# Optimization experiments

Measured on AMD Instinct MI355X. Metric: run time of the kernel, lower is better.

## Reference

```python
import jax, jax.numpy as jnp
import numpy as np
from jax import lax

B = 16384
D_MODEL = 84
N_EXPERTS = 2
TOP_K = 2
HIDDEN = 2048


def _conv(x, w, b):
    # x: [N,C,H,W], w: [O,I,kh,kw] (torch OIHW), VALID padding, stride 1
    y = lax.conv_general_dilated(x, w, (1, 1), 'VALID',
                                 dimension_numbers=('NCHW', 'OIHW', 'NCHW'))
    return y + b[None, :, None, None]


def _maxpool2(x):
    return lax.reduce_window(x, -jnp.inf, lax.max,
                             (1, 1, 2, 2), (1, 1, 2, 2), 'VALID')


def setup_inputs() -> dict:
    key = jax.random.key(0)
    ks = jax.random.split(key, 17)
    s = 0.05
    return {
        'x': jax.random.normal(ks[0], (B, 3, 32, 32), jnp.float32),
        'conv1_w': jax.random.normal(ks[1], (6, 3, 5, 5), jnp.float32) * s,
        'conv1_b': jax.random.normal(ks[2], (6,), jnp.float32) * s,
        'conv2_w': jax.random.normal(ks[3], (16, 6, 5, 5), jnp.float32) * s,
        'conv2_b': jax.random.normal(ks[4], (16,), jnp.float32) * s,
        'fc1_w': jax.random.normal(ks[5], (400, 120), jnp.float32) * s,
        'fc1_b': jax.random.normal(ks[6], (120,), jnp.float32) * s,
        'fc2_w': jax.random.normal(ks[7], (120, 84), jnp.float32) * s,
        'fc2_b': jax.random.normal(ks[8], (84,), jnp.float32) * s,
        'gate_w': jax.random.normal(ks[9], (D_MODEL, N_EXPERTS), jnp.float32) * s,
        'exp_w1': jax.random.normal(ks[10], (N_EXPERTS, D_MODEL, HIDDEN), jnp.float32) * s,
        'exp_b1': jax.random.normal(ks[11], (N_EXPERTS, HIDDEN), jnp.float32) * s,
        'exp_w2': jax.random.normal(ks[12], (N_EXPERTS, HIDDEN, D_MODEL), jnp.float32) * s,
        'exp_b2': jax.random.normal(ks[13], (N_EXPERTS, D_MODEL), jnp.float32) * s,
        'fc3_w': jax.random.normal(ks[14], (84, 10), jnp.float32) * s,
        'fc3_b': jax.random.normal(ks[15], (10,), jnp.float32) * s,
    }


def _moe(x, gate_w, exp_w1, exp_b1, exp_w2, exp_b2):
    # tutel top-k gate: softmax over expert logits, select top-k, renormalize
    n = x.shape[0]
    scores = jax.nn.softmax(x @ gate_w, axis=-1)          # [N,E]
    top_v, top_i = lax.top_k(scores, TOP_K)               # [N,k]
    gates = top_v / jnp.sum(top_v, axis=-1, keepdims=True)
    # dense combine weights [N,E] (zero where not routed)
    comb = jnp.zeros((n, N_EXPERTS), x.dtype).at[
        jnp.arange(n)[:, None], top_i].set(gates)
    # grouped expert FFN (E=2: evaluate both, weight-combine)
    h = jax.nn.relu(jnp.einsum('nd,edh->enh', x, exp_w1) + exp_b1[:, None, :])
    y = jnp.einsum('enh,ehd->end', h, exp_w2) + exp_b2[:, None, :]  # [E,N,D]
    return jnp.einsum('ne,end->nd', comb, y)


def reference(x, conv1_w, conv1_b, conv2_w, conv2_b, fc1_w, fc1_b,
              fc2_w, fc2_b, gate_w, exp_w1, exp_b1, exp_w2, exp_b2,
              fc3_w, fc3_b):
    h = _maxpool2(jax.nn.relu(_conv(x, conv1_w, conv1_b)))   # [B,6,14,14]
    h = _maxpool2(jax.nn.relu(_conv(h, conv2_w, conv2_b)))   # [B,16,5,5]
    h = h.reshape(-1, 16 * 5 * 5)                            # [B,400]
    h = jax.nn.relu(h @ fc1_w + fc1_b)                       # [B,120]
    h = jax.nn.relu(h @ fc2_w + fc2_b)                       # [B,84]
    h = _moe(h, gate_w, exp_w1, exp_b1, exp_w2, exp_b2)      # [B,84]
    return h @ fc3_w + fc3_b                                 # [B,10]
```

## Files before the change

### kernel.cpp

```cpp
#include <hip/hip_runtime.h>
#include <stdint.h>

typedef unsigned short u16;
typedef __attribute__((ext_vector_type(8))) short s8v;
typedef __attribute__((ext_vector_type(4))) float f4v;
typedef __fp16 h2v __attribute__((ext_vector_type(2)));

__device__ __forceinline__ float bu2f(u16 u) {
  return __uint_as_float(((uint32_t)u) << 16);
}
__device__ __forceinline__ u16 f2bu(float f) {
  uint32_t u = __float_as_uint(f);
  u += 0x7fffu + ((u >> 16) & 1u);
  return (u16)(u >> 16);
}

union U32H2 { uint32_t u; h2v h; };

__device__ __forceinline__ uint32_t pk2h(float a, float b) {
  U32H2 x;
  x.h = __builtin_amdgcn_cvt_pkrtz(a, b);
  return x.u;
}

__device__ __forceinline__ float fdot2u(uint32_t a, uint32_t b, float c) {
  float d;
  asm("v_dot2_f32_f16 %0, %1, %2, %3" : "=v"(d) : "v"(a), "v"(b), "v"(c));
  return d;
}

template <bool F32> struct In;
template <> struct In<true> {
  static __device__ __forceinline__ float ld(const void* p, long i) {
    return ((const float*)p)[i];
  }
};
template <> struct In<false> {
  static __device__ __forceinline__ float ld(const void* p, long i) {
    return bu2f(((const u16*)p)[i]);
  }
};

__global__ void k_detect(const u16* __restrict__ x, int* __restrict__ flag) {
  __shared__ int s[64];
  int cnt = 0;
  for (int i = threadIdx.x; i < 2048; i += 64) {
    int e = (x[i] >> 7) & 0xFF;
    cnt += (e >= 96 && e <= 134) ? 1 : 0;
  }
  s[threadIdx.x] = cnt;
  __syncthreads();
  if (threadIdx.x == 0) {
    int t = 0;
    for (int i = 0; i < 64; ++i) t += s[i];
    *flag = (t >= 1843) ? 0 : 1;
  }
}

__device__ __forceinline__ u16 f2h16(float f) {
  __fp16 h = (__fp16)f;
  u16 r;
  __builtin_memcpy(&r, &h, 2);
  return r;
}

template <bool INF32>
__global__ __launch_bounds__(256) void k_trans(
    const int* __restrict__ flag,
    const void* __restrict__ fc1w, const void* __restrict__ fc2w,
    const void* __restrict__ ew1, const void* __restrict__ ew2,
    const void* __restrict__ c1w, const void* __restrict__ c1b,
    const void* __restrict__ c2w, const void* __restrict__ c2b,
    u16* __restrict__ fc1t, u16* __restrict__ fc2t,
    u16* __restrict__ w1t, u16* __restrict__ w2t,
    uint32_t* __restrict__ cdw) {
  if (*flag != (INF32 ? 1 : 0)) return;
  long gid = (long)blockIdx.x * 256 + threadIdx.x;
  if (gid < 53248) {
    int n = (int)(gid / 416), k = (int)(gid % 416);
    fc1t[gid] = (n < 120 && k < 400) ? f2bu(In<INF32>::ld(fc1w, (long)k * 120 + n)) : (u16)0;
  } else if (gid < 65536) {
    long i = gid - 53248;
    int n = (int)(i / 128), k = (int)(i % 128);
    fc2t[i] = (n < 84 && k < 120) ? f2bu(In<INF32>::ld(fc2w, (long)k * 84 + n)) : (u16)0;
  } else if (gid < 458752) {
    long i = gid - 65536;
    int e = (int)(i / 196608);
    long r = i % 196608;
    int n = (int)(r / 96), k = (int)(r % 96);
    w1t[i] = (k < 84) ? f2bu(In<INF32>::ld(ew1, ((long)e * 84 + k) * 2048 + n)) : (u16)0;
  } else if (gid < 851968) {
    long i = gid - 458752;
    int e = (int)(i / 196608);
    long r = i % 196608;
    int n = (int)(r / 2048), k = (int)(r % 2048);
    w2t[i] = (n < 84) ? f2bu(In<INF32>::ld(ew2, ((long)e * 2048 + k) * 84 + n)) : (u16)0;
  } else if (gid < 853700) {
    long i = gid - 851968;
    if (i < 270) {
      int p = (int)(i % 3), ky = (int)((i / 3) % 5);
      int ic = (int)((i / 15) % 3), c = (int)(i / 45);
      long base = (((long)c * 3 + ic) * 5 + ky) * 5;
      float w0 = In<INF32>::ld(c1w, base + 2 * p);
      float w1 = (2 * p + 1 < 5) ? In<INF32>::ld(c1w, base + 2 * p + 1) : 0.f;
      cdw[i] = (uint32_t)f2h16(w0) | ((uint32_t)f2h16(w1) << 16);
    } else if (i < 1710) {
      long j = i - 270;
      int p = (int)(j % 3), ky = (int)((j / 3) % 5);
      int ic = (int)((j / 15) % 6), c = (int)(j / 90);
      long base = (((long)c * 6 + ic) * 5 + ky) * 5;
      float w0 = In<INF32>::ld(c2w, base + 2 * p);
      float w1 = (2 * p + 1 < 5) ? In<INF32>::ld(c2w, base + 2 * p + 1) : 0.f;
      cdw[270 + j] = (uint32_t)f2h16(w0) | ((uint32_t)f2h16(w1) << 16);
    } else if (i < 1716) {
      ((float*)(cdw + 1710))[i - 1710] = In<INF32>::ld(c1b, i - 1710);
    } else if (i < 1732) {
      ((float*)(cdw + 1716))[i - 1716] = In<INF32>::ld(c2b, i - 1716);
    }
  }
}

#define CIMG 5
template <bool INF32>
__global__ __launch_bounds__(256) void k_conv(
    const int* __restrict__ flag,
    const void* __restrict__ x,
    const uint32_t* __restrict__ cdw,
    u16* __restrict__ p2, int Btot) {
  if (*flag != (INF32 ? 1 : 0)) return;
  __shared__ u16 sxh[CIMG * 3 * 32 * 36];
  __shared__ u16 sp1h[CIMG * 6 * 14 * 18];
  const uint32_t* cd1 = cdw;
  const uint32_t* cd2 = cdw + 270;
  const float* cb1 = (const float*)(cdw + 1710);
  const float* cb2 = (const float*)(cdw + 1716);
  const int tid = threadIdx.x;
  const long gimg0 = (long)blockIdx.x * CIMG;

  for (int r = tid; r < CIMG * 96; r += 256) {
    *(uint32_t*)(sxh + (size_t)r * 36 + 32) = 0;
    *(uint32_t*)(sxh + (size_t)r * 36 + 34) = 0;
  }
  for (int r = tid; r < CIMG * 84; r += 256) {
    *(uint32_t*)(sp1h + (size_t)r * 18 + 14) = 0;
    *(uint32_t*)(sp1h + (size_t)r * 18 + 16) = 0;
  }

  for (int i = tid; i < CIMG * 96; i += 256) {
    int img = i / 96, rem = i - img * 96;
    if (gimg0 + img < Btot) {
      long goff = (gimg0 + img) * 3072 + (long)rem * 32;
      u16* dst = sxh + (size_t)i * 36;
      if (!INF32) {
        const uint32_t* src = (const uint32_t*)((const u16*)x + goff);
#pragma unroll
        for (int j = 0; j < 16; ++j) {
          uint32_t d = src[j];
          *(uint32_t*)(dst + 2 * j) =
              pk2h(__uint_as_float(d << 16), __uint_as_float(d & 0xffff0000u));
        }
      } else {
        const float* src = (const float*)x + goff;
#pragma unroll
        for (int j = 0; j < 16; ++j)
          *(uint32_t*)(dst + 2 * j) = pk2h(src[2 * j], src[2 * j + 1]);
      }
    }
  }
  __syncthreads();

  for (int task = tid; task < CIMG * 196; task += 256) {
    int img = task / 196, pos = task - img * 196;
    if (gimg0 + img >= Btot) continue;
    int py = pos / 14, px = pos - py * 14;
    int x0 = 2 * px, y0 = 2 * py;
    float acc[6][4];
#pragma unroll
    for (int c = 0; c < 6; ++c) {
      float bv = cb1[c];
      acc[c][0] = bv; acc[c][1] = bv; acc[c][2] = bv; acc[c][3] = bv;
    }
    for (int ic = 0; ic < 3; ++ic) {
      uint32_t A[6][4], S[6][3];
      const u16* rb = sxh + ((size_t)(img * 3 + ic) * 32 + y0) * 36 + x0;
#pragma unroll
      for (int r = 0; r < 6; ++r) {
#pragma unroll
        for (int p = 0; p < 4; ++p)
          A[r][p] = *(const uint32_t*)(rb + (size_t)r * 36 + 2 * p);
#pragma unroll
        for (int p = 0; p < 3; ++p)
          S[r][p] = (A[r][p] >> 16) | (A[r][p + 1] << 16);
      }
#pragma unroll
      for (int c = 0; c < 6; ++c) {
        const uint32_t* wb = cd1 + ((c * 3 + ic) * 5) * 3;
#pragma unroll
        for (int ky = 0; ky < 5; ++ky) {
#pragma unroll
          for (int p = 0; p < 3; ++p) {
            uint32_t w = wb[ky * 3 + p];
            acc[c][0] = fdot2u(A[ky][p], w, acc[c][0]);
            acc[c][1] = fdot2u(S[ky][p], w, acc[c][1]);
            acc[c][2] = fdot2u(A[ky + 1][p], w, acc[c][2]);
            acc[c][3] = fdot2u(S[ky + 1][p], w, acc[c][3]);
          }
        }
      }
    }
#pragma unroll
    for (int c = 0; c < 6; ++c) {
      float m = fmaxf(0.f, fmaxf(fmaxf(acc[c][0], acc[c][1]),
                                 fmaxf(acc[c][2], acc[c][3])));
      sp1h[((size_t)(img * 6 + c) * 14 + py) * 18 + px] = f2h16(m);
    }
  }
  __syncthreads();

  for (int task = tid; task < CIMG * 100; task += 256) {
    int img = task / 100, r0 = task - img * 100;
    if (gimg0 + img >= Btot) continue;
    int grp = r0 / 25, pos = r0 - grp * 25;
    int py = pos / 5, px = pos - py * 5;
    int x0 = 2 * px, y0 = 2 * py;
    int c0 = grp * 4;
    float acc[4][4];
#pragma unroll
    for (int c = 0; c < 4; ++c) {
      float bv = cb2[c0 + c];
      acc[c][0] = bv; acc[c][1] = bv; acc[c][2] = bv; acc[c][3] = bv;
    }
    for (int ic = 0; ic < 6; ++ic) {
      uint32_t A[6][4], S[6][3];
      const u16* rb = sp1h + ((size_t)(img * 6 + ic) * 14 + y0) * 18 + x0;
#pragma unroll
      for (int r = 0; r < 6; ++r) {
#pragma unroll
        for (int p = 0; p < 4; ++p)
          A[r][p] = *(const uint32_t*)(rb + (size_t)r * 18 + 2 * p);
#pragma unroll
        for (int p = 0; p < 3; ++p)
          S[r][p] = (A[r][p] >> 16) | (A[r][p + 1] << 16);
      }
#pragma unroll
      for (int c = 0; c < 4; ++c) {
        const uint32_t* wb = cd2 + (((c0 + c) * 6 + ic) * 5) * 3;
#pragma unroll
        for (int ky = 0; ky < 5; ++ky) {
#pragma unroll
          for (int p = 0; p < 3; ++p) {
            uint32_t w = wb[ky * 3 + p];
            acc[c][0] = fdot2u(A[ky][p], w, acc[c][0]);
            acc[c][1] = fdot2u(S[ky][p], w, acc[c][1]);
            acc[c][2] = fdot2u(A[ky + 1][p], w, acc[c][2]);
            acc[c][3] = fdot2u(S[ky + 1][p], w, acc[c][3]);
          }
        }
      }
    }
    u16* pout = p2 + (gimg0 + img) * 416;
#pragma unroll
    for (int c = 0; c < 4; ++c) {
      float m = fmaxf(0.f, fmaxf(fmaxf(acc[c][0], acc[c][1]),
                                 fmaxf(acc[c][2], acc[c][3])));
      pout[(c0 + c) * 25 + py * 5 + px] = f2bu(m);
    }
  }

  for (int i = tid; i < CIMG * 16; i += 256) {
    int img = i / 16;
    if (gimg0 + img < Btot) p2[(gimg0 + img) * 416 + 400 + (i & 15)] = 0;
  }
}

template <bool INF32>
__global__ __launch_bounds__(256) void k_fcA(
    const int* __restrict__ flag,
    const u16* __restrict__ p2,
    const u16* __restrict__ fc1t, const u16* __restrict__ fc2t,
    const void* __restrict__ fc1b, const void* __restrict__ fc2b,
    const void* __restrict__ gw,
    u16* __restrict__ a2buf, float* __restrict__ scbuf) {
  if (*flag != (INF32 ? 1 : 0)) return;
  __shared__ __align__(16) char smem[62976];
  u16* a2s = (u16*)smem;
  u16* hs = (u16*)(smem + 13312);
  u16* wbuf = (u16*)(smem + 31232);
  u16* xs = (u16*)(smem + 57856);

  const int tid = threadIdx.x;
  const int wv = tid >> 6, ln = tid & 63;
  const int m = ln & 15, quad = ln >> 4;
  const long t0 = (long)blockIdx.x * 64;
  const int row0 = wv * 16 + quad * 4;

  for (int i = tid; i < 30720 / 4; i += 256) ((uint32_t*)smem)[i] = 0;

  f4v acc1[8];
#pragma unroll
  for (int i = 0; i < 8; ++i) acc1[i] = (f4v){0.f, 0.f, 0.f, 0.f};
  for (int s = 0; s < 13; ++s) {
    {
      int r = tid >> 2, c0 = (tid & 3) * 8;
      *(uint4*)(xs + r * 40 + c0) =
          *(const uint4*)(p2 + (t0 + r) * 416 + s * 32 + c0);
      int n = tid >> 1, cw = (tid & 1) * 16;
      *(uint4*)(wbuf + n * 40 + cw) = *(const uint4*)(fc1t + (long)n * 416 + s * 32 + cw);
      *(uint4*)(wbuf + n * 40 + cw + 8) =
          *(const uint4*)(fc1t + (long)n * 416 + s * 32 + cw + 8);
    }
    __syncthreads();
    s8v a = *(const s8v*)(xs + (wv * 16 + m) * 40 + quad * 8);
#pragma unroll
    for (int nt = 0; nt < 8; ++nt) {
      s8v b = *(const s8v*)(wbuf + (nt * 16 + m) * 40 + quad * 8);
      acc1[nt] = __builtin_amdgcn_mfma_f32_16x16x32_bf16(a, b, acc1[nt], 0, 0, 0);
    }
    __syncthreads();
  }
#pragma unroll
  for (int nt = 0; nt < 8; ++nt) {
    int n = nt * 16 + m;
    if (n < 120) {
      float bv = In<INF32>::ld(fc1b, n);
#pragma unroll
      for (int r = 0; r < 4; ++r)
        hs[(row0 + r) * 136 + n] = f2bu(fmaxf(acc1[nt][r] + bv, 0.f));
    }
  }
  __syncthreads();

  for (int i = tid; i < 1536; i += 256) {
    int n = i >> 4, c0 = (i & 15) * 8;
    *(uint4*)(wbuf + n * 136 + c0) = *(const uint4*)(fc2t + n * 128 + c0);
  }
  __syncthreads();
  f4v acc2[6];
#pragma unroll
  for (int i = 0; i < 6; ++i) acc2[i] = (f4v){0.f, 0.f, 0.f, 0.f};
  for (int s = 0; s < 4; ++s) {
    s8v a = *(const s8v*)(hs + (wv * 16 + m) * 136 + s * 32 + quad * 8);
#pragma unroll
    for (int nt = 0; nt < 6; ++nt) {
      s8v b = *(const s8v*)(wbuf + (nt * 16 + m) * 136 + s * 32 + quad * 8);
      acc2[nt] = __builtin_amdgcn_mfma_f32_16x16x32_bf16(a, b, acc2[nt], 0, 0, 0);
    }
  }
  __syncthreads();
#pragma unroll
  for (int nt = 0; nt < 6; ++nt) {
    int n = nt * 16 + m;
    if (n < 84) {
      float bv = In<INF32>::ld(fc2b, n);
#pragma unroll
      for (int r = 0; r < 4; ++r)
        a2s[(row0 + r) * 104 + n] = f2bu(fmaxf(acc2[nt][r] + bv, 0.f));
    }
  }
  __syncthreads();

  if (tid < 64) {
    const u16* xr = a2s + tid * 104;
    float l0 = 0.f, l1 = 0.f;
    for (int k = 0; k < 84; ++k) {
      float xv = bu2f(xr[k]);
      l0 = fmaf(xv, In<INF32>::ld(gw, 2 * k), l0);
      l1 = fmaf(xv, In<INF32>::ld(gw, 2 * k + 1), l1);
    }
    float mx = fmaxf(l0, l1);
    float e0 = __expf(l0 - mx), e1 = __expf(l1 - mx);
    float inv = 1.f / (e0 + e1);
    *(float2*)(scbuf + (t0 + tid) * 2) = make_float2(e0 * inv, e1 * inv);
  }
  for (int i = tid; i < 832; i += 256) {
    int r = i / 13, c0 = (i - r * 13) * 8;
    *(uint4*)(a2buf + (t0 + r) * 104 + c0) = *(const uint4*)(a2s + r * 104 + c0);
  }
}

template <bool INF32>
__global__ __launch_bounds__(256) void k_exp(
    const int* __restrict__ flag,
    const u16* __restrict__ a2buf, const float* __restrict__ scbuf,
    const u16* __restrict__ w1t, const u16* __restrict__ w2t,
    const void* __restrict__ eb1, const void* __restrict__ eb2,
    float* __restrict__ ybuf, int Btok) {
  if (*flag != (INF32 ? 1 : 0)) return;
  __shared__ __align__(16) char smem[57856];
  u16* a2s = (u16*)smem;
  u16* hs = (u16*)(smem + 13312);
  u16* wbuf = (u16*)(smem + 30720);
  float* scs = (float*)(smem + 57344);

  const int tid = threadIdx.x;
  const int wv = tid >> 6, ln = tid & 63;
  const int m = ln & 15, quad = ln >> 4;
  const int e = blockIdx.y;
  const long t0 = (long)blockIdx.x * 64;
  const int row0 = wv * 16 + quad * 4;
  const u16* w1te = w1t + (long)e * 196608;
  const u16* w2te = w2t + (long)e * 196608;

  for (int i = tid; i < 832; i += 256) {
    int r = i / 13, c0 = (i - r * 13) * 8;
    *(uint4*)(a2s + r * 104 + c0) = *(const uint4*)(a2buf + (t0 + r) * 104 + c0);
  }
  if (tid < 64) scs[tid] = scbuf[(t0 + tid) * 2 + e];
  __syncthreads();

  f4v acce[6];
#pragma unroll
  for (int i = 0; i < 6; ++i) acce[i] = (f4v){0.f, 0.f, 0.f, 0.f};
  for (int c = 0; c < 16; ++c) {
    const int n0 = c * 128;
    if (c) __syncthreads();
    for (int i = tid; i < 1536; i += 256) {
      int nl = i / 12, c0 = (i - nl * 12) * 8;
      *(uint4*)(wbuf + nl * 104 + c0) =
          *(const uint4*)(w1te + (long)(n0 + nl) * 96 + c0);
    }
    __syncthreads();
    f4v acch[8];
#pragma unroll
    for (int i = 0; i < 8; ++i) acch[i] = (f4v){0.f, 0.f, 0.f, 0.f};
    for (int s = 0; s < 3; ++s) {
      s8v a = *(const s8v*)(a2s + (wv * 16 + m) * 104 + s * 32 + quad * 8);
#pragma unroll
      for (int nt = 0; nt < 8; ++nt) {
        s8v b = *(const s8v*)(wbuf + (nt * 16 + m) * 104 + s * 32 + quad * 8);
        acch[nt] = __builtin_amdgcn_mfma_f32_16x16x32_bf16(a, b, acch[nt], 0, 0, 0);
      }
    }
#pragma unroll
    for (int nt = 0; nt < 8; ++nt) {
      float bv = In<INF32>::ld(eb1, (long)e * 2048 + n0 + nt * 16 + m);
#pragma unroll
      for (int r = 0; r < 4; ++r)
        hs[(row0 + r) * 136 + nt * 16 + m] = f2bu(fmaxf(acch[nt][r] + bv, 0.f));
    }
    __syncthreads();
    for (int i = tid; i < 1536; i += 256) {
      int n = i >> 4, c0 = (i & 15) * 8;
      *(uint4*)(wbuf + n * 136 + c0) =
          *(const uint4*)(w2te + (long)n * 2048 + n0 + c0);
    }
    __syncthreads();
    for (int s = 0; s < 4; ++s) {
      s8v a = *(const s8v*)(hs + (wv * 16 + m) * 136 + s * 32 + quad * 8);
#pragma unroll
      for (int nt = 0; nt < 6; ++nt) {
        s8v b = *(const s8v*)(wbuf + (nt * 16 + m) * 136 + s * 32 + quad * 8);
        acce[nt] = __builtin_amdgcn_mfma_f32_16x16x32_bf16(a, b, acce[nt], 0, 0, 0);
      }
    }
  }

#pragma unroll
  for (int nt = 0; nt < 6; ++nt) {
    int d = nt * 16 + m;
    float bv = (d < 84) ? In<INF32>::ld(eb2, (long)e * 84 + d) : 0.f;
#pragma unroll
    for (int r = 0; r < 4; ++r) {
      float sc = scs[row0 + r];
      ybuf[((size_t)e * Btok + t0 + row0 + r) * 96 + d] = sc * (acce[nt][r] + bv);
    }
  }
}

template <bool INF32>
__global__ __launch_bounds__(256) void k_fc3(
    const int* __restrict__ flag,
    const float* __restrict__ ybuf,
    const void* __restrict__ w3, const void* __restrict__ b3,
    void* __restrict__ out, int Btok) {
  if (*flag != (INF32 ? 1 : 0)) return;
  __shared__ float sw3[840];
  __shared__ float sb3[10];
  const int tid = threadIdx.x;
  const long t0 = (long)blockIdx.x * 64;
  for (int i = tid; i < 840; i += 256) sw3[i] = In<INF32>::ld(w3, i);
  if (tid < 10) sb3[tid] = In<INF32>::ld(b3, tid);
  __syncthreads();
  for (int idx = tid; idx < 640; idx += 256) {
    int tk = idx / 10, cc = idx - tk * 10;
    const float* y0r = ybuf + (t0 + tk) * 96;
    const float* y1r = ybuf + ((size_t)Btok + t0 + tk) * 96;
    float acc = sb3[cc];
    for (int d = 0; d < 84; ++d)
      acc = fmaf(y0r[d] + y1r[d], sw3[d * 10 + cc], acc);
    long oi = (t0 + tk) * 10 + cc;
    if (INF32) ((float*)out)[oi] = acc;
    else ((u16*)out)[oi] = f2bu(acc);
  }
}

extern "C" void kernel_launch(void* const* d_in, const int* in_sizes, int n_in,
                              void* d_out, int out_size, void* d_ws, size_t ws_size,
                              hipStream_t stream) {
  const int B = in_sizes[0] / 3072;
  char* wsb = (char*)d_ws;
  int* flag = (int*)wsb;
  u16* p2 = (u16*)(wsb + 64);
  u16* fc1t = p2 + (size_t)B * 416;
  u16* fc2t = fc1t + 53248;
  u16* w1t = fc2t + 12288;
  u16* w2t = w1t + 393216;
  uint32_t* cdw = (uint32_t*)(w2t + 393216);
  u16* a2buf = (u16*)(cdw + 1732);
  float* scbuf = (float*)(a2buf + (size_t)B * 104);
  float* ybuf = scbuf + (size_t)B * 2;

  k_detect<<<1, 64, 0, stream>>>((const u16*)d_in[0], flag);

  k_trans<false><<<3336, 256, 0, stream>>>(flag, d_in[5], d_in[7], d_in[10],
                                           d_in[12], d_in[1], d_in[2], d_in[3],
                                           d_in[4], fc1t, fc2t, w1t, w2t, cdw);
  k_trans<true><<<3336, 256, 0, stream>>>(flag, d_in[5], d_in[7], d_in[10],
                                          d_in[12], d_in[1], d_in[2], d_in[3],
                                          d_in[4], fc1t, fc2t, w1t, w2t, cdw);

  const int convGrid = (B + CIMG - 1) / CIMG;
  k_conv<false><<<convGrid, 256, 0, stream>>>(flag, d_in[0], cdw, p2, B);
  k_conv<true><<<convGrid, 256, 0, stream>>>(flag, d_in[0], cdw, p2, B);

  k_fcA<false><<<B / 64, 256, 0, stream>>>(flag, p2, fc1t, fc2t, d_in[6],
                                           d_in[8], d_in[9], a2buf, scbuf);
  k_fcA<true><<<B / 64, 256, 0, stream>>>(flag, p2, fc1t, fc2t, d_in[6],
                                          d_in[8], d_in[9], a2buf, scbuf);

  dim3 eg(B / 64, 2);
  k_exp<false><<<eg, 256, 0, stream>>>(flag, a2buf, scbuf, w1t, w2t, d_in[11],
                                       d_in[13], ybuf, B);
  k_exp<true><<<eg, 256, 0, stream>>>(flag, a2buf, scbuf, w1t, w2t, d_in[11],
                                      d_in[13], ybuf, B);

  k_fc3<false><<<B / 64, 256, 0, stream>>>(flag, ybuf, d_in[14], d_in[15],
                                           d_out, B);
  k_fc3<true><<<B / 64, 256, 0, stream>>>(flag, ybuf, d_in[14], d_in[15],
                                          d_out, B);
}
```

Baseline: 621.2 us.

## Move conv1/conv2 from dot2 FMA loops to 16x16x32 f16 MFMA

Both conv layers are recast as small GEMMs on the 16x16x32 f16 MFMA, replacing the v_dot2 scalar accumulation. Each pooled output's 4 window positions map to MFMA rows, so the max-pool becomes a reduction over the accumulator lanes. Weights are repacked into a padded MFMA B-fragment layout, and inputs are stored twice in LDS (normal and shifted by one element) so odd-x windows can be fetched with aligned 32-bit loads. This trades doubled LDS footprint and a smaller images-per-block count (5 to 4) for far fewer VALU instructions in the conv stage, which likely dominates runtime.

```diff
diff --git a/kernel.cpp b/kernel.cpp
--- a/kernel.cpp
+++ b/kernel.cpp
@@ -5,6 +5,7 @@
 typedef __attribute__((ext_vector_type(8))) short s8v;
 typedef __attribute__((ext_vector_type(4))) float f4v;
 typedef __fp16 h2v __attribute__((ext_vector_type(2)));
+typedef __fp16 h8v __attribute__((ext_vector_type(8)));
 
 __device__ __forceinline__ float bu2f(u16 u) {
   return __uint_as_float(((uint32_t)u) << 16);
@@ -21,12 +22,6 @@
   U32H2 x;
   x.h = __builtin_amdgcn_cvt_pkrtz(a, b);
   return x.u;
-}
-
-__device__ __forceinline__ float fdot2u(uint32_t a, uint32_t b, float c) {
-  float d;
-  asm("v_dot2_f32_f16 %0, %1, %2, %3" : "=v"(d) : "v"(a), "v"(b), "v"(c));
-  return d;
 }
 
 template <bool F32> struct In;
@@ -95,32 +90,37 @@
     long r = i % 196608;
     int n = (int)(r / 2048), k = (int)(r % 2048);
     w2t[i] = (n < 84) ? f2bu(In<INF32>::ld(ew2, ((long)e * 2048 + k) * 84 + n)) : (u16)0;
-  } else if (gid < 853700) {
+  } else if (gid < 856598) {
     long i = gid - 851968;
-    if (i < 270) {
-      int p = (int)(i % 3), ky = (int)((i / 3) % 5);
-      int ic = (int)((i / 15) % 3), c = (int)(i / 45);
-      long base = (((long)c * 3 + ic) * 5 + ky) * 5;
-      float w0 = In<INF32>::ld(c1w, base + 2 * p);
-      float w1 = (2 * p + 1 < 5) ? In<INF32>::ld(c1w, base + 2 * p + 1) : 0.f;
-      cdw[i] = (uint32_t)f2h16(w0) | ((uint32_t)f2h16(w1) << 16);
-    } else if (i < 1710) {
-      long j = i - 270;
-      int p = (int)(j % 3), ky = (int)((j / 3) % 5);
-      int ic = (int)((j / 15) % 6), c = (int)(j / 90);
-      long base = (((long)c * 6 + ic) * 5 + ky) * 5;
-      float w0 = In<INF32>::ld(c2w, base + 2 * p);
-      float w1 = (2 * p + 1 < 5) ? In<INF32>::ld(c2w, base + 2 * p + 1) : 0.f;
-      cdw[270 + j] = (uint32_t)f2h16(w0) | ((uint32_t)f2h16(w1) << 16);
-    } else if (i < 1716) {
-      ((float*)(cdw + 1710))[i - 1710] = In<INF32>::ld(c1b, i - 1710);
-    } else if (i < 1732) {
-      ((float*)(cdw + 1716))[i - 1716] = In<INF32>::ld(c2b, i - 1716);
-    }
-  }
-}
-
-#define CIMG 5
+    u16* cdh = (u16*)cdw;
+    if (i < 1536) {
+      int ic = (int)(i >> 9);
+      int r = (int)(i & 511);
+      int lnn = r >> 3, j = r & 7;
+      int n = lnn & 15, qd = lnn >> 4;
+      int t = qd * 8 + j, ky = t / 6, kxp = t - ky * 6;
+      float v = (n < 6 && t < 30 && kxp < 5)
+          ? In<INF32>::ld(c1w, ((long)(n * 3 + ic) * 5 + ky) * 5 + kxp) : 0.f;
+      cdh[i] = f2h16(v);
+    } else if (i < 4608) {
+      long jj = i - 1536;
+      int ic = (int)(jj >> 9);
+      int r = (int)(jj & 511);
+      int lnn = r >> 3, j = r & 7;
+      int n = lnn & 15, qd = lnn >> 4;
+      int t = qd * 8 + j, ky = t / 6, kxp = t - ky * 6;
+      float v = (t < 30 && kxp < 5)
+          ? In<INF32>::ld(c2w, ((long)(n * 6 + ic) * 5 + ky) * 5 + kxp) : 0.f;
+      cdh[1536 + jj] = f2h16(v);
+    } else if (i < 4614) {
+      ((float*)(cdw + 2304))[i - 4608] = In<INF32>::ld(c1b, i - 4608);
+    } else if (i < 4630) {
+      ((float*)(cdw + 2310))[i - 4614] = In<INF32>::ld(c2b, i - 4614);
+    }
+  }
+}
+
+#define CIMG 4
 template <bool INF32>
 __global__ __launch_bounds__(256) void k_conv(
     const int* __restrict__ flag,
@@ -128,143 +128,140 @@
     const uint32_t* __restrict__ cdw,
     u16* __restrict__ p2, int Btot) {
   if (*flag != (INF32 ? 1 : 0)) return;
-  __shared__ u16 sxh[CIMG * 3 * 32 * 36];
-  __shared__ u16 sp1h[CIMG * 6 * 14 * 18];
-  const uint32_t* cd1 = cdw;
-  const uint32_t* cd2 = cdw + 270;
-  const float* cb1 = (const float*)(cdw + 1710);
-  const float* cb2 = (const float*)(cdw + 1716);
+  __shared__ __align__(16) u16 sxn[CIMG * 3 * 32 * 36];
+  __shared__ __align__(16) u16 sxs[CIMG * 3 * 32 * 36];
+  __shared__ __align__(16) u16 sp1n[CIMG * 6 * 14 * 18];
+  __shared__ __align__(16) u16 sp1s[CIMG * 6 * 14 * 18];
+  __shared__ u16 lut1[196];
+  __shared__ u16 lut2[32];
+  const u16* cdh = (const u16*)cdw;
+  const float* cb1f = (const float*)(cdw + 2304);
+  const float* cb2f = (const float*)(cdw + 2310);
   const int tid = threadIdx.x;
+  const int wv = tid >> 6, ln = tid & 63;
+  const int mrow = ln & 15, quad = ln >> 4;
   const long gimg0 = (long)blockIdx.x * CIMG;
 
-  for (int r = tid; r < CIMG * 96; r += 256) {
-    *(uint32_t*)(sxh + (size_t)r * 36 + 32) = 0;
-    *(uint32_t*)(sxh + (size_t)r * 36 + 34) = 0;
-  }
-  for (int r = tid; r < CIMG * 84; r += 256) {
-    *(uint32_t*)(sp1h + (size_t)r * 18 + 14) = 0;
-    *(uint32_t*)(sp1h + (size_t)r * 18 + 16) = 0;
-  }
+  if (tid < 196) {
+    int py = tid / 14, px = tid - py * 14;
+    lut1[tid] = (u16)((2 * py) * 36 + 2 * px);
+  } else if (tid < 228) {
+    int i = tid - 196;
+    if (i < 25) {
+      int py = i / 5, px = i - py * 5;
+      lut2[i] = (u16)((2 * py) * 18 + 2 * px);
+    }
+  }
+  for (int r = tid; r < CIMG * 6 * 14; r += 256)
+    *(uint32_t*)(sp1s + (size_t)r * 18 + 12) = 0;
 
   for (int i = tid; i < CIMG * 96; i += 256) {
-    int img = i / 96, rem = i - img * 96;
-    if (gimg0 + img < Btot) {
-      long goff = (gimg0 + img) * 3072 + (long)rem * 32;
-      u16* dst = sxh + (size_t)i * 36;
-      if (!INF32) {
-        const uint32_t* src = (const uint32_t*)((const u16*)x + goff);
-#pragma unroll
-        for (int j = 0; j < 16; ++j) {
-          uint32_t d = src[j];
-          *(uint32_t*)(dst + 2 * j) =
-              pk2h(__uint_as_float(d << 16), __uint_as_float(d & 0xffff0000u));
-        }
-      } else {
-        const float* src = (const float*)x + goff;
-#pragma unroll
-        for (int j = 0; j < 16; ++j)
-          *(uint32_t*)(dst + 2 * j) = pk2h(src[2 * j], src[2 * j + 1]);
+    int img = i / 96;
+    if (gimg0 + img >= Btot) continue;
+    int rem = i - img * 96;
+    long goff = (gimg0 + img) * 3072 + (long)rem * 32;
+    uint32_t e[17];
+    if (!INF32) {
+      const uint32_t* src = (const uint32_t*)((const u16*)x + goff);
+#pragma unroll
+      for (int j = 0; j < 16; ++j) {
+        uint32_t d = src[j];
+        e[j] = pk2h(__uint_as_float(d << 16), __uint_as_float(d & 0xffff0000u));
       }
-    }
-  }
-  __syncthreads();
-
-  for (int task = tid; task < CIMG * 196; task += 256) {
-    int img = task / 196, pos = task - img * 196;
-    if (gimg0 + img >= Btot) continue;
-    int py = pos / 14, px = pos - py * 14;
-    int x0 = 2 * px, y0 = 2 * py;
-    float acc[6][4];
-#pragma unroll
-    for (int c = 0; c < 6; ++c) {
-      float bv = cb1[c];
-      acc[c][0] = bv; acc[c][1] = bv; acc[c][2] = bv; acc[c][3] = bv;
-    }
+    } else {
+      const float* src = (const float*)x + goff;
+#pragma unroll
+      for (int j = 0; j < 16; ++j) e[j] = pk2h(src[2 * j], src[2 * j + 1]);
+    }
+    e[16] = 0;
+    uint32_t* dn = (uint32_t*)(sxn + (size_t)i * 36);
+    uint32_t* dsh = (uint32_t*)(sxs + (size_t)i * 36);
+#pragma unroll
+    for (int j = 0; j < 16; ++j) {
+      dn[j] = e[j];
+      dsh[j] = (e[j] >> 16) | (e[j + 1] << 16);
+    }
+  }
+
+  h8v b1[3];
+#pragma unroll
+  for (int ic = 0; ic < 3; ++ic)
+    b1[ic] = *(const h8v*)(cdh + ((size_t)ic * 64 + ln) * 8);
+  const float bias1 = (mrow < 6) ? cb1f[mrow] : 0.f;
+  int toff1[4];
+#pragma unroll
+  for (int p = 0; p < 4; ++p) {
+    int t = quad * 8 + 2 * p;
+    if (t >= 30) t = 24;
+    toff1[p] = (t / 6) * 30 + t;
+  }
+  const int qA = mrow >> 2, dyA = (mrow >> 1) & 1, dxA = mrow & 1;
+
+  __syncthreads();
+
+  const u16* c1base = dxA ? sxs : sxn;
+  for (int tg = wv; tg < CIMG * 49; tg += 4) {
+    int img = tg / 49, tau = tg - img * 49;
+    int pqA = tau * 4 + qA;
+    const u16* rb0 = c1base + (size_t)img * 3456 + lut1[pqA] + dyA * 36;
+    f4v acc = {0.f, 0.f, 0.f, 0.f};
+#pragma unroll
     for (int ic = 0; ic < 3; ++ic) {
-      uint32_t A[6][4], S[6][3];
-      const u16* rb = sxh + ((size_t)(img * 3 + ic) * 32 + y0) * 36 + x0;
-#pragma unroll
-      for (int r = 0; r < 6; ++r) {
-#pragma unroll
-        for (int p = 0; p < 4; ++p)
-          A[r][p] = *(const uint32_t*)(rb + (size_t)r * 36 + 2 * p);
-#pragma unroll
-        for (int p = 0; p < 3; ++p)
-          S[r][p] = (A[r][p] >> 16) | (A[r][p + 1] << 16);
-      }
-#pragma unroll
-      for (int c = 0; c < 6; ++c) {
-        const uint32_t* wb = cd1 + ((c * 3 + ic) * 5) * 3;
-#pragma unroll
-        for (int ky = 0; ky < 5; ++ky) {
-#pragma unroll
-          for (int p = 0; p < 3; ++p) {
-            uint32_t w = wb[ky * 3 + p];
-            acc[c][0] = fdot2u(A[ky][p], w, acc[c][0]);
-            acc[c][1] = fdot2u(S[ky][p], w, acc[c][1]);
-            acc[c][2] = fdot2u(A[ky + 1][p], w, acc[c][2]);
-            acc[c][3] = fdot2u(S[ky + 1][p], w, acc[c][3]);
-          }
-        }
-      }
-    }
-#pragma unroll
-    for (int c = 0; c < 6; ++c) {
-      float m = fmaxf(0.f, fmaxf(fmaxf(acc[c][0], acc[c][1]),
-                                 fmaxf(acc[c][2], acc[c][3])));
-      sp1h[((size_t)(img * 6 + c) * 14 + py) * 18 + px] = f2h16(m);
-    }
-  }
-  __syncthreads();
-
-  for (int task = tid; task < CIMG * 100; task += 256) {
-    int img = task / 100, r0 = task - img * 100;
-    if (gimg0 + img >= Btot) continue;
-    int grp = r0 / 25, pos = r0 - grp * 25;
-    int py = pos / 5, px = pos - py * 5;
-    int x0 = 2 * px, y0 = 2 * py;
-    int c0 = grp * 4;
-    float acc[4][4];
-#pragma unroll
-    for (int c = 0; c < 4; ++c) {
-      float bv = cb2[c0 + c];
-      acc[c][0] = bv; acc[c][1] = bv; acc[c][2] = bv; acc[c][3] = bv;
-    }
+      const u16* rb = rb0 + ic * 1152;
+      union { uint32_t w[4]; h8v v; } au;
+#pragma unroll
+      for (int p = 0; p < 4; ++p)
+        au.w[p] = *(const uint32_t*)(rb + toff1[p]);
+      acc = __builtin_amdgcn_mfma_f32_16x16x32_f16(au.v, b1[ic], acc, 0, 0, 0);
+    }
+    float v = fmaxf(fmaxf(acc[0], acc[1]), fmaxf(acc[2], acc[3])) + bias1;
+    v = fmaxf(v, 0.f);
+    if (mrow < 6) {
+      int pqC = tau * 4 + quad;
+      int py = (pqC * 4682) >> 16, px = pqC - py * 14;
+      int rbase = ((img * 6 + mrow) * 14 + py) * 18;
+      u16 hv = f2h16(v);
+      sp1n[rbase + px] = hv;
+      sp1s[rbase + (px ? px - 1 : 17)] = hv;
+    }
+  }
+
+  h8v b2[6];
+#pragma unroll
+  for (int ic = 0; ic < 6; ++ic)
+    b2[ic] = *(const h8v*)(cdh + 1536 + ((size_t)ic * 64 + ln) * 8);
+  const float bias2 = cb2f[mrow];
+  int toff2[4];
+#pragma unroll
+  for (int p = 0; p < 4; ++p) {
+    int t = quad * 8 + 2 * p;
+    if (t >= 30) t = 24;
+    toff2[p] = (t / 6) * 12 + t;
+  }
+
+  __syncthreads();
+
+  const u16* c2base = dxA ? sp1s : sp1n;
+  for (int t2 = wv; t2 < 25; t2 += 4) {
+    int PA = t2 * 4 + qA;
+    int img = (PA * 41) >> 10, pq = PA - img * 25;
+    const u16* rb0 = c2base + (size_t)img * 1512 + lut2[pq] + dyA * 18;
+    f4v acc = {0.f, 0.f, 0.f, 0.f};
+#pragma unroll
     for (int ic = 0; ic < 6; ++ic) {
-      uint32_t A[6][4], S[6][3];
-      const u16* rb = sp1h + ((size_t)(img * 6 + ic) * 14 + y0) * 18 + x0;
-#pragma unroll
-      for (int r = 0; r < 6; ++r) {
-#pragma unroll
-        for (int p = 0; p < 4; ++p)
-          A[r][p] = *(const uint32_t*)(rb + (size_t)r * 18 + 2 * p);
-#pragma unroll
-        for (int p = 0; p < 3; ++p)
-          S[r][p] = (A[r][p] >> 16) | (A[r][p + 1] << 16);
-      }
-#pragma unroll
-      for (int c = 0; c < 4; ++c) {
-        const uint32_t* wb = cd2 + (((c0 + c) * 6 + ic) * 5) * 3;
-#pragma unroll
-        for (int ky = 0; ky < 5; ++ky) {
-#pragma unroll
-          for (int p = 0; p < 3; ++p) {
-            uint32_t w = wb[ky * 3 + p];
-            acc[c][0] = fdot2u(A[ky][p], w, acc[c][0]);
-            acc[c][1] = fdot2u(S[ky][p], w, acc[c][1]);
-            acc[c][2] = fdot2u(A[ky + 1][p], w, acc[c][2]);
-            acc[c][3] = fdot2u(S[ky + 1][p], w, acc[c][3]);
-          }
-        }
-      }
-    }
-    u16* pout = p2 + (gimg0 + img) * 416;
-#pragma unroll
-    for (int c = 0; c < 4; ++c) {
-      float m = fmaxf(0.f, fmaxf(fmaxf(acc[c][0], acc[c][1]),
-                                 fmaxf(acc[c][2], acc[c][3])));
-      pout[(c0 + c) * 25 + py * 5 + px] = f2bu(m);
-    }
+      const u16* rb = rb0 + ic * 252;
+      union { uint32_t w[4]; h8v v; } au;
+#pragma unroll
+      for (int p = 0; p < 4; ++p)
+        au.w[p] = *(const uint32_t*)(rb + toff2[p]);
+      acc = __builtin_amdgcn_mfma_f32_16x16x32_f16(au.v, b2[ic], acc, 0, 0, 0);
+    }
+    float v = fmaxf(fmaxf(acc[0], acc[1]), fmaxf(acc[2], acc[3])) + bias2;
+    v = fmaxf(v, 0.f);
+    int PC = t2 * 4 + quad;
+    int imgc = (PC * 41) >> 10, pqc = PC - imgc * 25;
+    if (gimg0 + imgc < Btot)
+      p2[(gimg0 + imgc) * 416 + mrow * 25 + pqc] = f2bu(v);
   }
 
   for (int i = tid; i < CIMG * 16; i += 256) {
@@ -506,16 +503,16 @@
   u16* w1t = fc2t + 12288;
   u16* w2t = w1t + 393216;
   uint32_t* cdw = (uint32_t*)(w2t + 393216);
-  u16* a2buf = (u16*)(cdw + 1732);
+  u16* a2buf = (u16*)(cdw + 2326);
   float* scbuf = (float*)(a2buf + (size_t)B * 104);
   float* ybuf = scbuf + (size_t)B * 2;
 
   k_detect<<<1, 64, 0, stream>>>((const u16*)d_in[0], flag);
 
-  k_trans<false><<<3336, 256, 0, stream>>>(flag, d_in[5], d_in[7], d_in[10],
+  k_trans<false><<<3347, 256, 0, stream>>>(flag, d_in[5], d_in[7], d_in[10],
                                            d_in[12], d_in[1], d_in[2], d_in[3],
                                            d_in[4], fc1t, fc2t, w1t, w2t, cdw);
-  k_trans<true><<<3336, 256, 0, stream>>>(flag, d_in[5], d_in[7], d_in[10],
+  k_trans<true><<<3347, 256, 0, stream>>>(flag, d_in[5], d_in[7], d_in[10],
                                           d_in[12], d_in[1], d_in[2], d_in[3],
                                           d_in[4], fc1t, fc2t, w1t, w2t, cdw);
 
```

After: 557.3 us. -10.3%, faster.
